# Performance work log

Hardware: AMD Instinct MI355X
Metric: run time of the kernel (lower is better)

The kernel has to match this reference:

```python
import jax, jax.numpy as jnp
import numpy as np

N, E, D, H, O = 100000, 1600000, 256, 128, 64


def setup_inputs() -> dict:
    key = jax.random.key(0)
    ks = jax.random.split(key, 10)
    x = jax.random.normal(ks[0], (N, D), dtype=jnp.float32)
    # edges without self loops (original adds remaining self loops itself)
    row = jax.random.randint(ks[1], (E,), 0, N)
    off = jax.random.randint(ks[2], (E,), 1, N)
    col = (row + off) % N
    edge_index = jnp.stack([row, col]).astype(jnp.int64)
    # positive PPMI edge weights (stand-in for cached random-walk PPMI values)
    ppmi_edge_weight = jax.random.uniform(ks[3], (E,), dtype=jnp.float32, minval=0.1, maxval=1.0)
    # glorot-style weights (shared between GCN and PPMI branches, as in the module)
    W1 = jax.random.normal(ks[4], (D, H), dtype=jnp.float32) * np.sqrt(2.0 / (D + H))
    b1 = jnp.zeros((H,), dtype=jnp.float32)
    W2 = jax.random.normal(ks[5], (H, O), dtype=jnp.float32) * np.sqrt(2.0 / (H + O))
    b2 = jnp.zeros((O,), dtype=jnp.float32)
    dense_w = jax.random.normal(ks[6], (O, 1), dtype=jnp.float32) * np.sqrt(2.0 / (O + 1))
    dense_b = jnp.zeros((1,), dtype=jnp.float32)
    return {"x": x, "edge_index": edge_index, "ppmi_edge_weight": ppmi_edge_weight,
            "W1": W1, "b1": b1, "W2": W2, "b2": b2,
            "dense_w": dense_w, "dense_b": dense_b}


def _sym_norm(row, col, ew, n):
    # deg^-0.5[row] * w * deg^-0.5[col], deg from scatter-add over source index
    deg = jax.ops.segment_sum(ew, row, num_segments=n)
    dis = jnp.where(deg > 0, deg ** -0.5, 0.0)
    return dis[row] * ew * dis[col]


def _gconv(h, W, b, row, col, norm, n):
    hw = h @ W                              # [N, F_out]
    msg = norm[:, None] * hw[row]           # gather + scale, [E', F_out]
    return jax.ops.segment_sum(msg, col, num_segments=n) + b


def reference(x, edge_index, ppmi_edge_weight, W1, b1, W2, b2, dense_w, dense_b):
    n = x.shape[0]
    row = edge_index[0].astype(jnp.int32)
    col = edge_index[1].astype(jnp.int32)
    sl = jnp.arange(n, dtype=jnp.int32)
    row_sl = jnp.concatenate([row, sl])
    col_sl = jnp.concatenate([col, sl])
    ones_sl = jnp.ones((n,), dtype=x.dtype)

    # GCN branch: edge_weight = 1, plus self loops (fill_value = 1)
    gcn_ew = jnp.concatenate([jnp.ones((row.shape[0],), dtype=x.dtype), ones_sl])
    gnorm = _sym_norm(row_sl, col_sl, gcn_ew, n)
    g = jax.nn.relu(_gconv(x, W1, b1, row_sl, col_sl, gnorm, n))  # dropout p in eval -> identity
    g = _gconv(g, W2, b2, row_sl, col_sl, gnorm, n)

    # PPMI branch: precomputed positive weights, plus self loops
    ppmi_ew = jnp.concatenate([ppmi_edge_weight.astype(x.dtype), ones_sl])
    pnorm = _sym_norm(row_sl, col_sl, ppmi_ew, n)
    p = jax.nn.relu(_gconv(x, W1, b1, row_sl, col_sl, pnorm, n))
    p = _gconv(p, W2, b2, row_sl, col_sl, pnorm, n)

    stacked = jnp.stack([g, p], axis=1)                 # [N, 2, O]
    logits = stacked @ dense_w + dense_b                # [N, 2, 1]
    w = jax.nn.softmax(logits, axis=1)
    return jnp.sum(stacked * w, axis=1)                 # [N, O]
```

## Files before the change

### kernel.cpp

```cpp
#include <hip/hip_runtime.h>
#include <hip/hip_bf16.h>
#include <math.h>

#define DD 256
#define HH 128
#define OO 64

#define EPB 8192
#define BKT 512
#define AWIN 512

typedef __attribute__((ext_vector_type(8))) __bf16 bf16x8;
typedef __attribute__((ext_vector_type(4))) __bf16 bf16x4;
typedef __attribute__((ext_vector_type(4))) float f32x4;
typedef __attribute__((ext_vector_type(2))) float f32x2;
typedef __attribute__((ext_vector_type(4))) int i32x4;

__device__ inline float2 bf2_to_f2(unsigned u) {
    float2 r;
    r.x = __uint_as_float(u << 16);
    r.y = __uint_as_float(u & 0xffff0000u);
    return r;
}

__global__ void part_count_kernel(const int* __restrict__ row, const int* __restrict__ col,
                                  int e, int nb,
                                  int* __restrict__ cnt_col, int* __restrict__ cnt_row) {
    __shared__ int hc[256], hr[256];
    int t = threadIdx.x;
    if (t < 256) { hc[t] = 0; hr[t] = 0; }
    __syncthreads();
    int base = blockIdx.x * EPB;
    int lim  = min(EPB, e - base);
    for (int i = t; i < lim; i += 512) {
        atomicAdd(&hc[col[base + i] >> 9], 1);
        atomicAdd(&hr[row[base + i] >> 9], 1);
    }
    __syncthreads();
    if (t < nb) {
        cnt_col[blockIdx.x * nb + t] = hc[t];
        cnt_row[blockIdx.x * nb + t] = hr[t];
    }
}

__global__ void scan_blocks_kernel(const int* __restrict__ cnt_col, const int* __restrict__ cnt_row,
                                   int* __restrict__ base_col, int* __restrict__ base_row,
                                   int* __restrict__ tot_col, int* __restrict__ tot_row,
                                   int nblk, int nb) {
    __shared__ int s[256];
    int side = (blockIdx.x >= (unsigned)nb) ? 1 : 0;
    int b = blockIdx.x - side * nb;
    const int* cnt = side ? cnt_row : cnt_col;
    int* base = side ? base_row : base_col;
    int* tot  = side ? tot_row  : tot_col;
    int t = threadIdx.x;
    int v = (t < nblk) ? cnt[(size_t)t * nb + b] : 0;
    s[t] = v;
    __syncthreads();
    for (int off = 1; off < 256; off <<= 1) {
        int u = (t >= off) ? s[t - off] : 0;
        __syncthreads();
        s[t] += u;
        __syncthreads();
    }
    if (t < nblk) base[(size_t)t * nb + b] = s[t] - v;
    if (t == 255) tot[b] = s[255];
}

__global__ void add_bases_kernel(int* __restrict__ base_col, int* __restrict__ base_row,
                                 const int* __restrict__ tot_col, const int* __restrict__ tot_row,
                                 int* __restrict__ bb_col, int* __restrict__ bb_row,
                                 int* __restrict__ row_ptr, int n, int e, int nblk, int nb) {
    __shared__ int s[256];
    __shared__ int bbv;
    int side = (blockIdx.x >= (unsigned)nb) ? 1 : 0;
    int b = blockIdx.x - side * nb;
    const int* tot = side ? tot_row : tot_col;
    int* base = side ? base_row : base_col;
    int t = threadIdx.x;
    int v = (t < nb) ? tot[t] : 0;
    s[t] = v;
    __syncthreads();
    for (int off = 1; off < 256; off <<= 1) {
        int u = (t >= off) ? s[t - off] : 0;
        __syncthreads();
        s[t] += u;
        __syncthreads();
    }
    if (t == 0) {
        bbv = (b > 0) ? s[b - 1] : 0;
        (side ? bb_row : bb_col)[b] = bbv;
    }
    __syncthreads();
    int add = bbv;
    for (int j = t; j < nblk; j += blockDim.x) base[(size_t)j * nb + b] += add;
    if (blockIdx.x == 0 && t == 0) row_ptr[n] = e;
}

__global__ void part_scatter_kernel(const int* __restrict__ row, const int* __restrict__ col,
                                    const float* __restrict__ ppmi,
                                    const int* __restrict__ base_col, const int* __restrict__ base_row,
                                    int4* __restrict__ tmp_col, int2* __restrict__ tmp_row,
                                    int e, int nb) {
    __shared__ int cc[256], cr[256];
    int t = threadIdx.x;
    if (t < nb) {
        cc[t] = base_col[blockIdx.x * nb + t];
        cr[t] = base_row[blockIdx.x * nb + t];
    }
    __syncthreads();
    int base = blockIdx.x * EPB;
    int lim  = min(EPB, e - base);
    for (int i = t; i < lim; i += 512) {
        int r = row[base + i], c = col[base + i];
        int w = __float_as_int(ppmi[base + i]);
        int sc = atomicAdd(&cc[c >> 9], 1);
        tmp_col[sc] = make_int4(c, r, w, 0);
        int sr = atomicAdd(&cr[r >> 9], 1);
        tmp_row[sr] = make_int2(r, w);
    }
}

__global__ void deg_bucket_kernel(const int2* __restrict__ tmp_row,
                                  const int* __restrict__ bb_row, const int* __restrict__ tot_row,
                                  float2* __restrict__ dis, int n) {
    __shared__ float dg[BKT], dp[BKT];
    int t = threadIdx.x;
    dg[t] = 1.0f; dp[t] = 1.0f;
    __syncthreads();
    int b = blockIdx.x;
    int beg = bb_row[b], cnt = tot_row[b];
    for (int i = t; i < cnt; i += 512) {
        int2 cell = tmp_row[beg + i];
        int lr = cell.x & (BKT - 1);
        atomicAdd(&dg[lr], 1.0f);
        atomicAdd(&dp[lr], __int_as_float(cell.y));
    }
    __syncthreads();
    int g = (b << 9) + t;
    if (g < n) dis[g] = make_float2(rsqrtf(dg[t]), rsqrtf(dp[t]));
}

__launch_bounds__(512)
__global__ void csr_bucket_kernel(const int4* __restrict__ tmp_col,
                                  const int* __restrict__ bb_col, const int* __restrict__ tot_col,
                                  const float2* __restrict__ dis,
                                  int* __restrict__ row_ptr, int4* __restrict__ csr_meta, int n) {
    __shared__ int hist[BKT], s[BKT], cur[BKT];
    int t = threadIdx.x;
    hist[t] = 0;
    __syncthreads();
    int b = blockIdx.x;
    int beg = bb_col[b], cnt = tot_col[b];
    for (int i = t; i < cnt; i += BKT) atomicAdd(&hist[tmp_col[beg + i].x & (BKT - 1)], 1);
    __syncthreads();
    int own = hist[t];
    s[t] = own;
    __syncthreads();
    for (int off = 1; off < BKT; off <<= 1) {
        int v = (t >= off) ? s[t - off] : 0;
        __syncthreads();
        s[t] += v;
        __syncthreads();
    }
    int gslot = beg + s[t] - own;
    cur[t] = gslot;
    int gc = (b << 9) + t;
    if (gc < n) row_ptr[gc] = gslot;
    __syncthreads();
    for (int i = t; i < cnt; i += BKT) {
        int4 cell = tmp_col[beg + i];
        int lc = cell.x & (BKT - 1);
        int slot = atomicAdd(&cur[lc], 1);
        int r = cell.y;
        float w = __int_as_float(cell.z);
        float2 d = dis[r];
        csr_meta[slot] = make_int4(r, __float_as_int(d.x), __float_as_int(d.y * w), 0);
    }
}

__global__ void conv_w_kernel(const float* __restrict__ W, __bf16* __restrict__ Bh,
                              __bf16* __restrict__ Bl, int K, int N) {
    int i = blockIdx.x * blockDim.x + threadIdx.x;
    if (i >= K * N) return;
    int k = i / N, nn = i % N;
    float v = W[i];
    __bf16 h = (__bf16)v;
    Bh[(size_t)nn * K + k] = h;
    Bl[(size_t)nn * K + k] = (__bf16)(v - (float)h);
}

template<int BN, typename OT, bool ILV>
__launch_bounds__(256, 2)
__global__ void mfma_gemm_reg_kernel(const float* __restrict__ A,
                                     const __bf16* __restrict__ Bth, const __bf16* __restrict__ Btl,
                                     OT* __restrict__ C, int M, int K, int nHalf) {
    constexpr int NT = BN / 16;
    const int tid  = threadIdx.x;
    const int wave = tid >> 6;
    const int lane = tid & 63;
    const int quad = lane >> 4;
    const int l16  = lane & 15;
    const int row0 = blockIdx.x * 128 + wave * 32;

    f32x4 acc[2][NT] = {};

    for (int k0 = 0; k0 < K; k0 += 32) {
        bf16x8 bh[NT], bl[NT];
#pragma unroll
        for (int j = 0; j < NT; ++j) {
            size_t boff = (size_t)(j * 16 + l16) * K + k0 + quad * 8;
            bh[j] = *(const bf16x8*)(Bth + boff);
            bl[j] = *(const bf16x8*)(Btl + boff);
        }
#pragma unroll
        for (int i = 0; i < 2; ++i) {
            int gr = row0 + i * 16 + l16;
            float4 v0 = make_float4(0.f, 0.f, 0.f, 0.f);
            float4 v1 = make_float4(0.f, 0.f, 0.f, 0.f);
            if (gr < M) {
                const float* ap = A + (size_t)gr * K + k0 + quad * 8;
                v0 = *(const float4*)ap;
                v1 = *(const float4*)(ap + 4);
            }
            float vv0 = v0.x, vv1 = v0.y, vv2 = v0.z, vv3 = v0.w;
            float vv4 = v1.x, vv5 = v1.y, vv6 = v1.z, vv7 = v1.w;
            __bf16 h0 = (__bf16)vv0, h1 = (__bf16)vv1, h2 = (__bf16)vv2, h3 = (__bf16)vv3;
            __bf16 h4 = (__bf16)vv4, h5 = (__bf16)vv5, h6 = (__bf16)vv6, h7 = (__bf16)vv7;
            bf16x8 ah = (bf16x8){h0, h1, h2, h3, h4, h5, h6, h7};
            bf16x8 al = (bf16x8){(__bf16)(vv0 - (float)h0), (__bf16)(vv1 - (float)h1),
                                 (__bf16)(vv2 - (float)h2), (__bf16)(vv3 - (float)h3),
                                 (__bf16)(vv4 - (float)h4), (__bf16)(vv5 - (float)h5),
                                 (__bf16)(vv6 - (float)h6), (__bf16)(vv7 - (float)h7)};
#pragma unroll
            for (int j = 0; j < NT; ++j) {
                acc[i][j] = __builtin_amdgcn_mfma_f32_16x16x32_bf16(ah, bh[j], acc[i][j], 0, 0, 0);
                acc[i][j] = __builtin_amdgcn_mfma_f32_16x16x32_bf16(ah, bl[j], acc[i][j], 0, 0, 0);
                acc[i][j] = __builtin_amdgcn_mfma_f32_16x16x32_bf16(al, bh[j], acc[i][j], 0, 0, 0);
            }
        }
    }

#pragma unroll
    for (int i = 0; i < 2; ++i) {
#pragma unroll
        for (int rg = 0; rg < 4; ++rg) {
            int gr = row0 + i * 16 + quad * 4 + rg;
            if (gr < M) {
                if constexpr (ILV) {
                    int s = (gr >= nHalf) ? 1 : 0;
                    size_t base = (size_t)(gr - s * nHalf) * (BN * 2) + s;
#pragma unroll
                    for (int j = 0; j < NT; ++j)
                        C[base + (size_t)(j * 16 + l16) * 2] = (OT)acc[i][j][rg];
                } else {
#pragma unroll
                    for (int j = 0; j < NT; ++j)
                        C[(size_t)gr * BN + j * 16 + l16] = (OT)acc[i][j][rg];
                }
            }
        }
    }
}

__global__ void agg1_pull_kernel(const int* __restrict__ row_ptr, const int4* __restrict__ meta,
                                 const __bf16* __restrict__ hw1,
                                 const float2* __restrict__ dis,
                                 const float* __restrict__ b1,
                                 float* __restrict__ g_out, float* __restrict__ p_out, int n) {
    __shared__ i32x4 sm[AWIN];
    const int tid  = threadIdx.x;
    const int wave = tid >> 6;
    const int lane = tid & 63;
    const int c0   = blockIdx.x * 4;
    const int c    = c0 + wave;
    const int beg0 = row_ptr[c0];
    const int end3 = row_ptr[min(c0 + 4, n)];
    int beg = 0, end = 0;
    if (c < n) { beg = row_ptr[c]; end = row_ptr[c + 1]; }
    const int f2 = lane * 2;
    float sgx = 0.f, sgy = 0.f, spx = 0.f, spy = 0.f;

    for (int w = beg0; w < end3; w += AWIN) {
        const int cnt = min(AWIN, end3 - w);
        __syncthreads();
        for (int i = tid; i < cnt; i += 256)
            sm[i] = __builtin_nontemporal_load((const i32x4*)meta + w + i);
        __syncthreads();
        int t = max(beg, w);
        const int hi = min(end, w + cnt);
        for (; t + 8 <= hi; t += 8) {
            i32x4 m[8];
#pragma unroll
            for (int q = 0; q < 8; ++q) m[q] = sm[t - w + q];
            unsigned u[8];
#pragma unroll
            for (int q = 0; q < 8; ++q)
                u[q] = *(const unsigned*)(hw1 + ((size_t)(unsigned)m[q].x << 7) + f2);
#pragma unroll
            for (int q = 0; q < 8; ++q) {
                float2 h = bf2_to_f2(u[q]);
                float wg = __uint_as_float((unsigned)m[q].y);
                float wp = __uint_as_float((unsigned)m[q].z);
                sgx += wg * h.x; sgy += wg * h.y;
                spx += wp * h.x; spy += wp * h.y;
            }
        }
        if (t + 4 <= hi) {
            i32x4 m[4];
#pragma unroll
            for (int q = 0; q < 4; ++q) m[q] = sm[t - w + q];
            unsigned u[4];
#pragma unroll
            for (int q = 0; q < 4; ++q)
                u[q] = *(const unsigned*)(hw1 + ((size_t)(unsigned)m[q].x << 7) + f2);
#pragma unroll
            for (int q = 0; q < 4; ++q) {
                float2 h = bf2_to_f2(u[q]);
                float wg = __uint_as_float((unsigned)m[q].y);
                float wp = __uint_as_float((unsigned)m[q].z);
                sgx += wg * h.x; sgy += wg * h.y;
                spx += wp * h.x; spy += wp * h.y;
            }
            t += 4;
        }
        for (; t < hi; ++t) {
            i32x4 m0 = sm[t - w];
            float2 h0 = bf2_to_f2(*(const unsigned*)(hw1 + ((size_t)(unsigned)m0.x << 7) + f2));
            float wg0 = __uint_as_float((unsigned)m0.y);
            float wp0 = __uint_as_float((unsigned)m0.z);
            sgx += wg0 * h0.x; sgy += wg0 * h0.y;
            spx += wp0 * h0.x; spy += wp0 * h0.y;
        }
    }

    if (c < n) {
        float2 d = dis[c];
        size_t idx = ((size_t)c << 7) + f2;
        float2 hs = bf2_to_f2(*(const unsigned*)(hw1 + idx));
        float2 bv = *(const float2*)(b1 + f2);
        float gx = d.x * sgx + d.x * d.x * hs.x + bv.x;
        float gy = d.x * sgy + d.x * d.x * hs.y + bv.y;
        float px = d.y * spx + d.y * d.y * hs.x + bv.x;
        float py = d.y * spy + d.y * d.y * hs.y + bv.y;
        f32x2 go, po;
        go[0] = gx > 0.f ? gx : 0.f;  go[1] = gy > 0.f ? gy : 0.f;
        po[0] = px > 0.f ? px : 0.f;  po[1] = py > 0.f ? py : 0.f;
        __builtin_nontemporal_store(go, (f32x2*)(g_out + idx));
        __builtin_nontemporal_store(po, (f32x2*)(p_out + idx));
    }
}

__global__ void agg2_final_kernel(const int* __restrict__ row_ptr, const int4* __restrict__ meta,
                                  const __bf16* __restrict__ hw2i,
                                  const float2* __restrict__ dis,
                                  const float* __restrict__ b2,
                                  const float* __restrict__ dense_w, const float* __restrict__ dense_b,
                                  float* __restrict__ out, int n) {
    __shared__ i32x4 sm[AWIN];
    const int tid  = threadIdx.x;
    const int wave = tid >> 6;
    const int f    = tid & 63;
    const int c0   = blockIdx.x * 4;
    const int c    = c0 + wave;
    const int beg0 = row_ptr[c0];
    const int end3 = row_ptr[min(c0 + 4, n)];
    int beg = 0, end = 0;
    if (c < n) { beg = row_ptr[c]; end = row_ptr[c + 1]; }
    const int f2 = f * 2;
    float sg = 0.f, sp = 0.f;

    for (int w = beg0; w < end3; w += AWIN) {
        const int cnt = min(AWIN, end3 - w);
        __syncthreads();
        for (int i = tid; i < cnt; i += 256)
            sm[i] = __builtin_nontemporal_load((const i32x4*)meta + w + i);
        __syncthreads();
        int t = max(beg, w);
        const int hi = min(end, w + cnt);
        for (; t + 8 <= hi; t += 8) {
            i32x4 m[8];
#pragma unroll
            for (int q = 0; q < 8; ++q) m[q] = sm[t - w + q];
            unsigned u[8];
#pragma unroll
            for (int q = 0; q < 8; ++q)
                u[q] = *(const unsigned*)(hw2i + ((size_t)(unsigned)m[q].x << 7) + f2);
#pragma unroll
            for (int q = 0; q < 8; ++q) {
                float2 g0 = bf2_to_f2(u[q]);
                sg += __uint_as_float((unsigned)m[q].y) * g0.x;
                sp += __uint_as_float((unsigned)m[q].z) * g0.y;
            }
        }
        if (t + 4 <= hi) {
            i32x4 m[4];
#pragma unroll
            for (int q = 0; q < 4; ++q) m[q] = sm[t - w + q];
            unsigned u[4];
#pragma unroll
            for (int q = 0; q < 4; ++q)
                u[q] = *(const unsigned*)(hw2i + ((size_t)(unsigned)m[q].x << 7) + f2);
#pragma unroll
            for (int q = 0; q < 4; ++q) {
                float2 g0 = bf2_to_f2(u[q]);
                sg += __uint_as_float((unsigned)m[q].y) * g0.x;
                sp += __uint_as_float((unsigned)m[q].z) * g0.y;
            }
            t += 4;
        }
        for (; t < hi; ++t) {
            i32x4 m0 = sm[t - w];
            float2 g0 = bf2_to_f2(*(const unsigned*)(hw2i + ((size_t)(unsigned)m0.x << 7) + f2));
            sg += __uint_as_float((unsigned)m0.y) * g0.x;
            sp += __uint_as_float((unsigned)m0.z) * g0.y;
        }
    }

    if (c < n) {
        float2 d = dis[c];
        float2 gps = bf2_to_f2(*(const unsigned*)(hw2i + ((size_t)c << 7) + f2));
        float bb = b2[f];
        float gv = d.x * sg + d.x * d.x * gps.x + bb;
        float pv = d.y * sp + d.y * d.y * gps.y + bb;
        float dwv = dense_w[f];
        float lg = gv * dwv, lp = pv * dwv;
#pragma unroll
        for (int off = 32; off > 0; off >>= 1) {
            lg += __shfl_xor(lg, off, 64);
            lp += __shfl_xor(lp, off, 64);
        }
        lg += dense_b[0];
        lp += dense_b[0];
        float m  = fmaxf(lg, lp);
        float eg = expf(lg - m), ep = expf(lp - m);
        float wgt = eg / (eg + ep);
        __builtin_nontemporal_store(wgt * gv + (1.0f - wgt) * pv, out + (size_t)c * OO + f);
    }
}

extern "C" void kernel_launch(void* const* d_in, const int* in_sizes, int n_in,
                              void* d_out, int out_size, void* d_ws, size_t ws_size,
                              hipStream_t stream) {
    const float* x    = (const float*)d_in[0];
    const int*   ei   = (const int*)d_in[1];
    const float* ppmi = (const float*)d_in[2];
    const float* W1   = (const float*)d_in[3];
    const float* b1   = (const float*)d_in[4];
    const float* W2   = (const float*)d_in[5];
    const float* b2   = (const float*)d_in[6];
    const float* dw   = (const float*)d_in[7];
    const float* db   = (const float*)d_in[8];
    float* out = (float*)d_out;

    const int n = in_sizes[0] / DD;
    const int e = in_sizes[2];
    const int* row = ei;
    const int* col = ei + e;

    const int nb   = (n + BKT - 1) / BKT;
    const int nblk = (e + EPB - 1) / EPB;

    float* ws      = (float*)d_ws;
    float2* dis    = (float2*)ws;
    __bf16* hw1    = (__bf16*)(ws + 2 * (size_t)n);
    float* g1      = (float*)(hw1 + (size_t)n * HH);
    float* p1      = g1 + (size_t)n * HH;
    int4* csr_meta = (int4*)(p1 + (size_t)n * HH);
    __bf16* bt1h   = (__bf16*)(csr_meta + e);
    __bf16* bt1l   = bt1h + (size_t)DD * HH;
    __bf16* bt2h   = bt1l + (size_t)DD * HH;
    __bf16* bt2l   = bt2h + (size_t)HH * OO;
    int* row_ptr   = (int*)(bt2l + (size_t)HH * OO);
    int* cnt_col   = row_ptr + (n + 1);
    int* base_col  = cnt_col + (size_t)nblk * nb;
    int* cnt_row   = base_col + (size_t)nblk * nb;
    int* base_row  = cnt_row + (size_t)nblk * nb;
    int* bb_col    = base_row + (size_t)nblk * nb;
    int* tot_col   = bb_col + nb;
    int* bb_row    = tot_col + nb;
    int* tot_row   = bb_row + nb;
    int4* tmp_col  = (int4*)g1;
    int2* tmp_row  = (int2*)p1;
    __bf16* hw2i   = hw1;

    const int T = 256;

    part_count_kernel<<<nblk, 512, 0, stream>>>(row, col, e, nb, cnt_col, cnt_row);
    scan_blocks_kernel<<<2 * nb, T, 0, stream>>>(cnt_col, cnt_row, base_col, base_row,
                                                 tot_col, tot_row, nblk, nb);
    add_bases_kernel<<<2 * nb, T, 0, stream>>>(base_col, base_row, tot_col, tot_row,
                                               bb_col, bb_row, row_ptr, n, e, nblk, nb);
    part_scatter_kernel<<<nblk, 512, 0, stream>>>(row, col, ppmi, base_col, base_row,
                                                  tmp_col, tmp_row, e, nb);
    deg_bucket_kernel<<<nb, 512, 0, stream>>>(tmp_row, bb_row, tot_row, dis, n);
    csr_bucket_kernel<<<nb, BKT, 0, stream>>>(tmp_col, bb_col, tot_col, dis,
                                              row_ptr, csr_meta, n);

    conv_w_kernel<<<(DD * HH + T - 1) / T, T, 0, stream>>>(W1, bt1h, bt1l, DD, HH);
    conv_w_kernel<<<(HH * OO + T - 1) / T, T, 0, stream>>>(W2, bt2h, bt2l, HH, OO);

    mfma_gemm_reg_kernel<HH, __bf16, false><<<(n + 127) / 128, 256, 0, stream>>>(
        x, bt1h, bt1l, hw1, n, DD, 0);
    agg1_pull_kernel<<<(n + 3) / 4, 256, 0, stream>>>(row_ptr, csr_meta, hw1, dis, b1, g1, p1, n);
    mfma_gemm_reg_kernel<OO, __bf16, true><<<(2 * n + 127) / 128, 256, 0, stream>>>(
        g1, bt2h, bt2l, hw2i, 2 * n, HH, n);
    agg2_final_kernel<<<(n + 3) / 4, 256, 0, stream>>>(row_ptr, csr_meta, hw2i, dis,
                                                       b2, dw, db, out, n);
}
```

Baseline: 549.2 us.

## Split GEMM column tiles across waves, prefetch A tiles, raise occupancy

The first GEMM now splits the 128 output columns across two waves per 32-row tile, halving accumulator and B-fragment registers. Launch bounds rise to allow four blocks per CU. The A-row loads for the next k-step are software-prefetched into registers so global latency overlaps the MFMA work. Row-bounds checks are removed, which relies on n and 2n being multiples of 32. The A tile is now loaded twice (once per column split) and conversion work is duplicated.

```diff
diff --git a/kernel.cpp b/kernel.cpp
--- a/kernel.cpp
+++ b/kernel.cpp
@@ -190,41 +190,50 @@
     Bl[(size_t)nn * K + k] = (__bf16)(v - (float)h);
 }
 
-template<int BN, typename OT, bool ILV>
-__launch_bounds__(256, 2)
+template<int BN, int CS, typename OT, bool ILV>
+__launch_bounds__(256, 4)
 __global__ void mfma_gemm_reg_kernel(const float* __restrict__ A,
                                      const __bf16* __restrict__ Bth, const __bf16* __restrict__ Btl,
                                      OT* __restrict__ C, int M, int K, int nHalf) {
-    constexpr int NT = BN / 16;
+    constexpr int NT = BN / CS / 16;
     const int tid  = threadIdx.x;
     const int wave = tid >> 6;
     const int lane = tid & 63;
     const int quad = lane >> 4;
     const int l16  = lane & 15;
-    const int row0 = blockIdx.x * 128 + wave * 32;
+    const int gw   = blockIdx.x * 4 + wave;
+    const int row0 = (gw / CS) * 32;
+    const int cb   = (gw % CS) * (BN / CS);
+    if (row0 >= M) return;
 
     f32x4 acc[2][NT] = {};
 
+    const float* ap0 = A + (size_t)(row0 + l16) * K + quad * 8;
+    const float* ap1 = A + (size_t)(row0 + 16 + l16) * K + quad * 8;
+
+    float4 a0[2][2];
+    a0[0][0] = *(const float4*)ap0;  a0[0][1] = *(const float4*)(ap0 + 4);
+    a0[1][0] = *(const float4*)ap1;  a0[1][1] = *(const float4*)(ap1 + 4);
+
     for (int k0 = 0; k0 < K; k0 += 32) {
+        float4 a1[2][2];
+        if (k0 + 32 < K) {
+            a1[0][0] = *(const float4*)(ap0 + k0 + 32);
+            a1[0][1] = *(const float4*)(ap0 + k0 + 36);
+            a1[1][0] = *(const float4*)(ap1 + k0 + 32);
+            a1[1][1] = *(const float4*)(ap1 + k0 + 36);
+        }
         bf16x8 bh[NT], bl[NT];
 #pragma unroll
         for (int j = 0; j < NT; ++j) {
-            size_t boff = (size_t)(j * 16 + l16) * K + k0 + quad * 8;
+            size_t boff = (size_t)(cb + j * 16 + l16) * K + k0 + quad * 8;
             bh[j] = *(const bf16x8*)(Bth + boff);
             bl[j] = *(const bf16x8*)(Btl + boff);
         }
 #pragma unroll
         for (int i = 0; i < 2; ++i) {
-            int gr = row0 + i * 16 + l16;
-            float4 v0 = make_float4(0.f, 0.f, 0.f, 0.f);
-            float4 v1 = make_float4(0.f, 0.f, 0.f, 0.f);
-            if (gr < M) {
-                const float* ap = A + (size_t)gr * K + k0 + quad * 8;
-                v0 = *(const float4*)ap;
-                v1 = *(const float4*)(ap + 4);
-            }
-            float vv0 = v0.x, vv1 = v0.y, vv2 = v0.z, vv3 = v0.w;
-            float vv4 = v1.x, vv5 = v1.y, vv6 = v1.z, vv7 = v1.w;
+            float vv0 = a0[i][0].x, vv1 = a0[i][0].y, vv2 = a0[i][0].z, vv3 = a0[i][0].w;
+            float vv4 = a0[i][1].x, vv5 = a0[i][1].y, vv6 = a0[i][1].z, vv7 = a0[i][1].w;
             __bf16 h0 = (__bf16)vv0, h1 = (__bf16)vv1, h2 = (__bf16)vv2, h3 = (__bf16)vv3;
             __bf16 h4 = (__bf16)vv4, h5 = (__bf16)vv5, h6 = (__bf16)vv6, h7 = (__bf16)vv7;
             bf16x8 ah = (bf16x8){h0, h1, h2, h3, h4, h5, h6, h7};
@@ -239,6 +248,10 @@
                 acc[i][j] = __builtin_amdgcn_mfma_f32_16x16x32_bf16(al, bh[j], acc[i][j], 0, 0, 0);
             }
         }
+        if (k0 + 32 < K) {
+            a0[0][0] = a1[0][0]; a0[0][1] = a1[0][1];
+            a0[1][0] = a1[1][0]; a0[1][1] = a1[1][1];
+        }
     }
 
 #pragma unroll
@@ -246,18 +259,16 @@
 #pragma unroll
         for (int rg = 0; rg < 4; ++rg) {
             int gr = row0 + i * 16 + quad * 4 + rg;
-            if (gr < M) {
-                if constexpr (ILV) {
-                    int s = (gr >= nHalf) ? 1 : 0;
-                    size_t base = (size_t)(gr - s * nHalf) * (BN * 2) + s;
-#pragma unroll
-                    for (int j = 0; j < NT; ++j)
-                        C[base + (size_t)(j * 16 + l16) * 2] = (OT)acc[i][j][rg];
-                } else {
-#pragma unroll
-                    for (int j = 0; j < NT; ++j)
-                        C[(size_t)gr * BN + j * 16 + l16] = (OT)acc[i][j][rg];
-                }
+            if constexpr (ILV) {
+                int s = (gr >= nHalf) ? 1 : 0;
+                size_t base = (size_t)(gr - s * nHalf) * (BN * 2) + s;
+#pragma unroll
+                for (int j = 0; j < NT; ++j)
+                    C[base + (size_t)(cb + j * 16 + l16) * 2] = (OT)acc[i][j][rg];
+            } else {
+#pragma unroll
+                for (int j = 0; j < NT; ++j)
+                    C[(size_t)gr * BN + cb + j * 16 + l16] = (OT)acc[i][j][rg];
             }
         }
     }
@@ -500,11 +511,17 @@
     conv_w_kernel<<<(DD * HH + T - 1) / T, T, 0, stream>>>(W1, bt1h, bt1l, DD, HH);
     conv_w_kernel<<<(HH * OO + T - 1) / T, T, 0, stream>>>(W2, bt2h, bt2l, HH, OO);
 
-    mfma_gemm_reg_kernel<HH, __bf16, false><<<(n + 127) / 128, 256, 0, stream>>>(
-        x, bt1h, bt1l, hw1, n, DD, 0);
+    {
+        int waves1 = (n / 32) * 2;
+        mfma_gemm_reg_kernel<HH, 2, __bf16, false><<<(waves1 + 3) / 4, 256, 0, stream>>>(
+            x, bt1h, bt1l, hw1, n, DD, 0);
+    }
     agg1_pull_kernel<<<(n + 3) / 4, 256, 0, stream>>>(row_ptr, csr_meta, hw1, dis, b1, g1, p1, n);
-    mfma_gemm_reg_kernel<OO, __bf16, true><<<(2 * n + 127) / 128, 256, 0, stream>>>(
-        g1, bt2h, bt2l, hw2i, 2 * n, HH, n);
+    {
+        int waves2 = (2 * n) / 32;
+        mfma_gemm_reg_kernel<OO, 1, __bf16, true><<<(waves2 + 3) / 4, 256, 0, stream>>>(
+            g1, bt2h, bt2l, hw2i, 2 * n, HH, n);
+    }
     agg2_final_kernel<<<(n + 3) / 4, 256, 0, stream>>>(row_ptr, csr_meta, hw2i, dis,
                                                        b2, dw, db, out, n);
 }
```

After: 547.1 us. No clear change (-0.4%).
